# Kernel tuning notes

Measured on AMD Instinct MI355X. Metric: run time of the kernel, lower is better.

The kernel has to match this reference:

```python
import jax, jax.numpy as jnp
import numpy as np

WS = 16  # window_size

def _conv1x1(x, w, b):
    # x: [n,c,h,w], w: [out,in], b: [out]
    return jnp.einsum('nchw,oc->nohw', x, w) + b[None, :, None, None]

def _se_attention(x, w1, b1, w2, b2):
    # global avg pool -> conv -> relu -> conv -> sigmoid; returns [n,C,1,1]
    p = x.mean(axis=(2, 3), keepdims=True)
    h = jax.nn.relu(_conv1x1(p, w1, b1))
    return jax.nn.sigmoid(_conv1x1(h, w2, b2))

def setup_inputs() -> dict:
    key = jax.random.key(0)
    ks = jax.random.split(key, 13)
    B, C, H, W = 8, 96, 256, 256
    Cr = C // 3
    s = 0.02
    return {
        'x': jax.random.normal(ks[0], (B, C, H, W), jnp.float32),
        'w_real': jax.random.normal(ks[1], (C, C), jnp.float32) * s,
        'b_real': jnp.zeros((C,), jnp.float32),
        'w_imag': jax.random.normal(ks[2], (C, C), jnp.float32) * s,
        'b_imag': jnp.zeros((C,), jnp.float32),
        'car_w1': jax.random.normal(ks[3], (Cr, C), jnp.float32) * s,
        'car_b1': jnp.zeros((Cr,), jnp.float32),
        'car_w2': jax.random.normal(ks[4], (C, Cr), jnp.float32) * s,
        'car_b2': jnp.zeros((C,), jnp.float32),
        'cai_w1': jax.random.normal(ks[5], (Cr, C), jnp.float32) * s,
        'cai_b1': jnp.zeros((Cr,), jnp.float32),
        'cai_w2': jax.random.normal(ks[6], (C, Cr), jnp.float32) * s,
        'cai_b2': jnp.zeros((C,), jnp.float32),
    }

def reference(x, w_real, b_real, w_imag, b_imag,
              car_w1, car_b1, car_w2, car_b2,
              cai_w1, cai_b1, cai_w2, cai_b2):
    B, C, H, W = x.shape
    nH, nW = H // WS, W // WS
    # window partition: [B,C,H,W] -> [B*nH*nW, C, WS, WS]
    xw = x.reshape(B, C, nH, WS, nW, WS)
    xw = xw.transpose(0, 2, 4, 1, 3, 5).reshape(-1, C, WS, WS)
    # 2D FFT per window, ortho norm
    x_fft = jnp.fft.fft2(xw, norm='ortho')
    real_conv = _conv1x1(jnp.real(x_fft), w_real, b_real)
    imag_conv = _conv1x1(jnp.imag(x_fft), w_imag, b_imag)
    real_att = _se_attention(real_conv, car_w1, car_b1, car_w2, car_b2)
    imag_att = _se_attention(imag_conv, cai_w1, cai_b1, cai_w2, cai_b2)
    real_conv = real_conv * (1.0 + real_att)
    imag_conv = imag_conv * (1.0 + imag_att)
    x_fft_enh = jax.lax.complex(real_conv, imag_conv)
    x_ifft = jnp.real(jnp.fft.ifft2(x_fft_enh, norm='ortho'))
    # window merge: [B*nH*nW, C, WS, WS] -> [B,C,H,W]
    out = x_ifft.reshape(B, nH, nW, C, WS, WS)
    out = out.transpose(0, 3, 1, 4, 2, 5).reshape(B, C, H, W)
    return out
```

## Files before the change

### kernel.cpp

```cpp
#include <hip/hip_runtime.h>
#include <hip/hip_bf16.h>
#include <math.h>

#define NWIN 2048

typedef __bf16 v8bf __attribute__((ext_vector_type(8)));
typedef float  v4f  __attribute__((ext_vector_type(4)));

__global__ __launch_bounds__(128) void se_alpha_kernel(
    const float* __restrict__ x,
    const float* __restrict__ w_real, const float* __restrict__ b_real,
    const float* __restrict__ car_w1, const float* __restrict__ car_b1,
    const float* __restrict__ car_w2, const float* __restrict__ car_b2,
    const float* __restrict__ b_imag,
    const float* __restrict__ cai_w1, const float* __restrict__ cai_b1,
    const float* __restrict__ cai_w2, const float* __restrict__ cai_b2,
    float* __restrict__ alpha, float* __restrict__ beta)
{
    __shared__ float wr_s[96 * 97];
    __shared__ float w1_s[32 * 97];
    __shared__ float w2_s[96 * 33];
    __shared__ float x0_s[96 * 17];
    __shared__ float pr_s[16 * 97];
    __shared__ float h1_s[16 * 33];
    const int t = threadIdx.x;
    const int blkid = blockIdx.x;

    if (blkid < 128) {
        const int b = blkid >> 4, wh = blkid & 15;
        for (int idx = t; idx < 96 * 96; idx += 128) {
            int o = idx / 96, c = idx - o * 96;
            wr_s[o * 97 + c] = w_real[idx];
        }
        for (int idx = t; idx < 32 * 96; idx += 128) {
            int j = idx / 96, c = idx - j * 96;
            w1_s[j * 97 + c] = car_w1[idx];
        }
        for (int idx = t; idx < 96 * 32; idx += 128) {
            int o = idx >> 5, j = idx & 31;
            w2_s[o * 33 + j] = car_w2[idx];
        }
        for (int idx = t; idx < 96 * 16; idx += 128) {
            int c = idx >> 4, w = idx & 15;
            x0_s[c * 17 + w] = x[(((size_t)(b * 96 + c)) * 256 + wh * 16) * 256 + w * 16];
        }
        __syncthreads();
        #pragma unroll
        for (int i = 0; i < 12; ++i) {
            int p = t + i * 128;
            int o = p >> 4, w = p & 15;
            float acc = 0.f;
            #pragma unroll 4
            for (int c = 0; c < 96; ++c) acc += wr_s[o * 97 + c] * x0_s[c * 17 + w];
            pr_s[w * 97 + o] = acc * (1.0f / 16.0f) + b_real[o];
        }
        __syncthreads();
        #pragma unroll
        for (int i = 0; i < 4; ++i) {
            int p = t + i * 128;
            int j = p >> 4, w = p & 15;
            float acc = car_b1[j];
            #pragma unroll 4
            for (int o = 0; o < 96; ++o) acc += w1_s[j * 97 + o] * pr_s[w * 97 + o];
            h1_s[w * 33 + j] = fmaxf(acc, 0.f);
        }
        __syncthreads();
        #pragma unroll
        for (int i = 0; i < 12; ++i) {
            int p = t + i * 128;
            int o = p >> 4, w = p & 15;
            float acc = car_b2[o];
            #pragma unroll
            for (int j = 0; j < 32; ++j) acc += w2_s[o * 33 + j] * h1_s[w * 33 + j];
            int n = (blkid << 4) | w;
            alpha[(size_t)n * 96 + o] = 1.f + 1.f / (1.f + __expf(-acc));
        }
    } else {
        if (t < 32) {
            float acc = cai_b1[t];
            for (int o = 0; o < 96; ++o) acc += cai_w1[t * 96 + o] * b_imag[o];
            h1_s[t] = fmaxf(acc, 0.f);
        }
        __syncthreads();
        if (t < 96) {
            float acc = cai_b2[t];
            for (int j = 0; j < 32; ++j) acc += cai_w2[t * 32 + j] * h1_s[j];
            beta[t] = 1.f + 1.f / (1.f + __expf(-acc));
        }
    }
}

__global__ __launch_bounds__(1024, 4) void wfca_main_kernel(
    const float* __restrict__ x,
    const float* __restrict__ w_real, const float* __restrict__ w_imag,
    const float* __restrict__ b_real,
    const float* __restrict__ alpha, const float* __restrict__ beta,
    float* __restrict__ out)
{
    __shared__ __bf16 wr_s[96 * 104];
    __shared__ __bf16 wi_s[96 * 104];
    __shared__ float  xf[3][32 * 256];
    __shared__ float  alpha_s[768];

    const int t    = threadIdx.x;
    const int blk  = blockIdx.x;
    const int b    = blk >> 5;
    const int wh   = (blk >> 1) & 15;
    const int ch   = blk & 1;

    const int lane = t & 63;
    const int l16  = lane & 15;
    const int quad = lane >> 4;
    const int wv   = t >> 6;
    const int r2m  = wv >> 3;
    const int wm   = wv & 7;

    const int pxq = (wm * 16 + l16) ^ ((quad & 1) << 4);
    const int pfq = (wm * 16 + ((16 - l16) & 15)) ^ ((quad & 1) << 4);

    auto issue = [&](int rp_, int k_, int buf_) {
        const int hl = rp_;
        const int hh = (rp_ == 0) ? 8 : 16 - rp_;
        #pragma unroll
        for (int u = 0; u < 2; ++u) {
            const int c    = 2 * wv + u;
            const int swz  = ((c >> 3) & 1) << 4;
            const int row  = (lane >> 5) ? hh : hl;
            const int colg = (4 * (lane & 31)) ^ swz;
            const float* g = x + (((size_t)(b * 96 + k_ * 32 + c)) << 16)
                           + (size_t)(wh * 16 + row) * 256 + ch * 128 + colg;
            float* l = &xf[buf_][c * 256];
            __builtin_amdgcn_global_load_lds(
                (const __attribute__((address_space(1))) float*)g,
                (__attribute__((address_space(3))) float*)l, 16, 0, 0);
        }
    };

    {
        float wrv[9], wiv[9], btv[9];
        #pragma unroll
        for (int r = 0; r < 9; ++r) {
            int idx = t + r * 1024;
            wrv[r] = w_real[idx];
            wiv[r] = w_imag[idx];
            btv[r] = beta[idx / 96];
        }
        #pragma unroll
        for (int r = 0; r < 9; ++r) {
            int idx = t + r * 1024;
            int o = idx / 96, c = idx - o * 96;
            wr_s[o * 104 + c] = (__bf16)(0.5f * wrv[r]);
            wi_s[o * 104 + c] = (__bf16)(0.5f * btv[r] * wiv[r]);
        }
    }
    if (t < 768) {
        int w = t / 96, o = t - w * 96;
        alpha_s[t] = alpha[(size_t)(b * 256 + wh * 16 + ch * 8 + w) * 96 + o];
    }
    float brv[6];
    #pragma unroll
    for (int n = 0; n < 6; ++n) brv[n] = b_real[n * 16 + l16];
    __syncthreads();

    issue(0, 0, 0);
    issue(0, 1, 1);

    for (int rp = 0; rp < 8; ++rp) {
        const int h_lo   = rp;
        const int h_hi   = (rp == 0) ? 8 : 16 - rp;
        const int h_out  = r2m ? h_hi : h_lo;
        const int flipr2 = (rp == 0) ? r2m : 1 - r2m;

        float af[6];
        v4f acc[6];
        #pragma unroll
        for (int n = 0; n < 6; ++n) {
            af[n]  = alpha_s[wm * 96 + n * 16 + l16];
            acc[n] = v4f{0.f, 0.f, 0.f, 0.f};
        }
        #pragma unroll
        for (int k = 0; k < 3; ++k) {
            if (rp == 7 && k == 2)      asm volatile("s_waitcnt vmcnt(0)" ::: "memory");
            else if (rp == 0 || k == 2) asm volatile("s_waitcnt vmcnt(2)" ::: "memory");
            else                        asm volatile("s_waitcnt vmcnt(8)" ::: "memory");
            __builtin_amdgcn_s_barrier();
            __builtin_amdgcn_sched_barrier(0);

            if (k == 0)      issue(rp, 2, 2);
            else if (k == 1) { if (rp < 7) issue(rp + 1, 0, 0); }
            else             { if (rp < 7) issue(rp + 1, 1, 1); }

            const float* xk = xf[k];
            float fxv[8], ffv[8];
            #pragma unroll
            for (int j = 0; j < 8; ++j) {
                fxv[j] = xk[(quad * 8 + j) * 256 + r2m * 128 + pxq];
                ffv[j] = xk[(quad * 8 + j) * 256 + flipr2 * 128 + pfq];
            }
            v8bf a_x, a_f, a_fn;
            #pragma unroll
            for (int j = 0; j < 8; ++j) {
                a_x[j]  = (__bf16)fxv[j];
                a_f[j]  = (__bf16)ffv[j];
                a_fn[j] = (__bf16)(-ffv[j]);
            }
            const int c0 = k * 32;
            #pragma unroll
            for (int n = 0; n < 6; ++n) {
                v8bf bwr = *(const v8bf*)&wr_s[(n * 16 + l16) * 104 + c0 + quad * 8];
                v8bf bwi = *(const v8bf*)&wi_s[(n * 16 + l16) * 104 + c0 + quad * 8];
                acc[n] = __builtin_amdgcn_mfma_f32_16x16x32_bf16(a_x,  bwi, acc[n], 0, 0, 0);
                acc[n] = __builtin_amdgcn_mfma_f32_16x16x32_bf16(a_fn, bwi, acc[n], 0, 0, 0);
                v4f utmp = __builtin_amdgcn_mfma_f32_16x16x32_bf16(
                               a_x, bwr, v4f{0.f, 0.f, 0.f, 0.f}, 0, 0, 0);
                utmp = __builtin_amdgcn_mfma_f32_16x16x32_bf16(a_f, bwr, utmp, 0, 0, 0);
                #pragma unroll
                for (int r = 0; r < 4; ++r) acc[n][r] += af[n] * utmp[r];
            }
        }

        {
            #pragma unroll
            for (int n = 0; n < 6; ++n) {
                const int o = n * 16 + l16;
                v4f v = acc[n];
                if (h_out == 0 && quad == 0) {
                    v[0] += 16.f * af[n] * brv[n];
                }
                size_t idx = (((size_t)(b * 96 + o)) * 256 + wh * 16 + h_out) * 256
                             + ch * 128 + wm * 16 + quad * 4;
                *(v4f*)(out + idx) = v;
            }
        }
    }
}

extern "C" void kernel_launch(void* const* d_in, const int* in_sizes, int n_in,
                              void* d_out, int out_size, void* d_ws, size_t ws_size,
                              hipStream_t stream) {
    const float* x      = (const float*)d_in[0];
    const float* w_real = (const float*)d_in[1];
    const float* b_real = (const float*)d_in[2];
    const float* w_imag = (const float*)d_in[3];
    const float* b_imag = (const float*)d_in[4];
    const float* car_w1 = (const float*)d_in[5];
    const float* car_b1 = (const float*)d_in[6];
    const float* car_w2 = (const float*)d_in[7];
    const float* car_b2 = (const float*)d_in[8];
    const float* cai_w1 = (const float*)d_in[9];
    const float* cai_b1 = (const float*)d_in[10];
    const float* cai_w2 = (const float*)d_in[11];
    const float* cai_b2 = (const float*)d_in[12];
    float* out = (float*)d_out;

    float* alpha = (float*)d_ws;
    float* beta  = alpha + NWIN * 96;

    se_alpha_kernel<<<129, 128, 0, stream>>>(
        x, w_real, b_real, car_w1, car_b1, car_w2, car_b2,
        b_imag, cai_w1, cai_b1, cai_w2, cai_b2, alpha, beta);

    wfca_main_kernel<<<256, 1024, 0, stream>>>(
        x, w_real, w_imag, b_real, alpha, beta, out);
}
```

Measured before the change: 419.2 us.

## Split main kernel into 512 half-size blocks with double-buffered LDS staging

Each block now covers 4 windows (a quarter row of windows) with 512 threads instead of 8 windows with 1024 threads, doubling the grid to 512 blocks. The LDS staging drops from triple-buffered 256-column tiles to double-buffered 128-column tiles. The load schedule becomes a simple one-ahead pipeline with a fresh swizzle and updated waitcnts. This aims to raise occupancy and balance work across CUs by cutting per-block LDS. The cost is shallower prefetch and weight tables loaded into LDS twice as many times.

```diff
diff --git a/kernel.cpp b/kernel.cpp
--- a/kernel.cpp
+++ b/kernel.cpp
@@ -90,7 +90,7 @@
     }
 }
 
-__global__ __launch_bounds__(1024, 4) void wfca_main_kernel(
+__global__ __launch_bounds__(512, 4) void wfca_main_kernel(
     const float* __restrict__ x,
     const float* __restrict__ w_real, const float* __restrict__ w_imag,
     const float* __restrict__ b_real,
@@ -99,63 +99,63 @@
 {
     __shared__ __bf16 wr_s[96 * 104];
     __shared__ __bf16 wi_s[96 * 104];
-    __shared__ float  xf[3][32 * 256];
-    __shared__ float  alpha_s[768];
+    __shared__ float  xf[2][32 * 128];
+    __shared__ float  alpha_s[384];
 
     const int t    = threadIdx.x;
     const int blk  = blockIdx.x;
-    const int b    = blk >> 5;
-    const int wh   = (blk >> 1) & 15;
-    const int ch   = blk & 1;
+    const int b    = blk >> 6;
+    const int wh   = (blk >> 2) & 15;
+    const int cq   = blk & 3;
 
     const int lane = t & 63;
     const int l16  = lane & 15;
     const int quad = lane >> 4;
     const int wv   = t >> 6;
-    const int r2m  = wv >> 3;
-    const int wm   = wv & 7;
-
-    const int pxq = (wm * 16 + l16) ^ ((quad & 1) << 4);
-    const int pfq = (wm * 16 + ((16 - l16) & 15)) ^ ((quad & 1) << 4);
+    const int r2m  = wv >> 2;
+    const int wm   = wv & 3;
+
+    const int pxq = (wm * 16 + l16) ^ (quad << 4);
+    const int pfq = (wm * 16 + ((16 - l16) & 15)) ^ (quad << 4);
 
     auto issue = [&](int rp_, int k_, int buf_) {
         const int hl = rp_;
         const int hh = (rp_ == 0) ? 8 : 16 - rp_;
         #pragma unroll
         for (int u = 0; u < 2; ++u) {
-            const int c    = 2 * wv + u;
-            const int swz  = ((c >> 3) & 1) << 4;
-            const int row  = (lane >> 5) ? hh : hl;
-            const int colg = (4 * (lane & 31)) ^ swz;
+            const int c    = 4 * wv + 2 * u + (lane >> 5);
+            const int row  = ((lane & 31) >> 4) ? hh : hl;
+            const int colg = (4 * (lane & 15)) ^ (((c >> 3) & 3) << 4);
             const float* g = x + (((size_t)(b * 96 + k_ * 32 + c)) << 16)
-                           + (size_t)(wh * 16 + row) * 256 + ch * 128 + colg;
-            float* l = &xf[buf_][c * 256];
+                           + (size_t)(wh * 16 + row) * 256 + cq * 64 + colg;
+            float* l = &xf[buf_][(4 * wv + 2 * u) * 128];
             __builtin_amdgcn_global_load_lds(
                 (const __attribute__((address_space(1))) float*)g,
                 (__attribute__((address_space(3))) float*)l, 16, 0, 0);
         }
     };
 
-    {
+    #pragma unroll
+    for (int gph = 0; gph < 2; ++gph) {
         float wrv[9], wiv[9], btv[9];
         #pragma unroll
         for (int r = 0; r < 9; ++r) {
-            int idx = t + r * 1024;
+            int idx = t + (gph * 9 + r) * 512;
             wrv[r] = w_real[idx];
             wiv[r] = w_imag[idx];
             btv[r] = beta[idx / 96];
         }
         #pragma unroll
         for (int r = 0; r < 9; ++r) {
-            int idx = t + r * 1024;
+            int idx = t + (gph * 9 + r) * 512;
             int o = idx / 96, c = idx - o * 96;
             wr_s[o * 104 + c] = (__bf16)(0.5f * wrv[r]);
             wi_s[o * 104 + c] = (__bf16)(0.5f * btv[r] * wiv[r]);
         }
     }
-    if (t < 768) {
+    if (t < 384) {
         int w = t / 96, o = t - w * 96;
-        alpha_s[t] = alpha[(size_t)(b * 256 + wh * 16 + ch * 8 + w) * 96 + o];
+        alpha_s[t] = alpha[(size_t)(b * 256 + wh * 16 + cq * 4 + w) * 96 + o];
     }
     float brv[6];
     #pragma unroll
@@ -163,7 +163,6 @@
     __syncthreads();
 
     issue(0, 0, 0);
-    issue(0, 1, 1);
 
     for (int rp = 0; rp < 8; ++rp) {
         const int h_lo   = rp;
@@ -180,22 +179,23 @@
         }
         #pragma unroll
         for (int k = 0; k < 3; ++k) {
-            if (rp == 7 && k == 2)      asm volatile("s_waitcnt vmcnt(0)" ::: "memory");
-            else if (rp == 0 || k == 2) asm volatile("s_waitcnt vmcnt(2)" ::: "memory");
-            else                        asm volatile("s_waitcnt vmcnt(8)" ::: "memory");
+            const int p = rp * 3 + k;
+            if (k == 0 && rp > 0) asm volatile("s_waitcnt vmcnt(6)" ::: "memory");
+            else                  asm volatile("s_waitcnt vmcnt(0)" ::: "memory");
             __builtin_amdgcn_s_barrier();
             __builtin_amdgcn_sched_barrier(0);
 
-            if (k == 0)      issue(rp, 2, 2);
-            else if (k == 1) { if (rp < 7) issue(rp + 1, 0, 0); }
-            else             { if (rp < 7) issue(rp + 1, 1, 1); }
-
-            const float* xk = xf[k];
+            if (p < 23) {
+                int pn = p + 1;
+                issue(pn / 3, pn % 3, pn & 1);
+            }
+
+            const float* xk = xf[p & 1];
             float fxv[8], ffv[8];
             #pragma unroll
             for (int j = 0; j < 8; ++j) {
-                fxv[j] = xk[(quad * 8 + j) * 256 + r2m * 128 + pxq];
-                ffv[j] = xk[(quad * 8 + j) * 256 + flipr2 * 128 + pfq];
+                fxv[j] = xk[(quad * 8 + j) * 128 + r2m * 64 + pxq];
+                ffv[j] = xk[(quad * 8 + j) * 128 + flipr2 * 64 + pfq];
             }
             v8bf a_x, a_f, a_fn;
             #pragma unroll
@@ -228,7 +228,7 @@
                     v[0] += 16.f * af[n] * brv[n];
                 }
                 size_t idx = (((size_t)(b * 96 + o)) * 256 + wh * 16 + h_out) * 256
-                             + ch * 128 + wm * 16 + quad * 4;
+                             + cq * 64 + wm * 16 + quad * 4;
                 *(v4f*)(out + idx) = v;
             }
         }
@@ -260,6 +260,6 @@
         x, w_real, b_real, car_w1, car_b1, car_w2, car_b2,
         b_imag, cai_w1, cai_b1, cai_w2, cai_b2, alpha, beta);
 
-    wfca_main_kernel<<<256, 1024, 0, stream>>>(
+    wfca_main_kernel<<<512, 512, 0, stream>>>(
         x, w_real, w_imag, b_real, alpha, beta, out);
 }
```

Result: no change. 426.3 us (+1.7%).
